# Optimization experiments

Hardware: AMD Instinct MI355X
Metric: run time of the kernel (lower is better)

## Reference

```python
import jax, jax.numpy as jnp
import numpy as np

B, S, D, H = 2, 2048, 2048, 16
DPH = D // H  # 128


def setup_inputs() -> dict:
    key = jax.random.key(0)
    k1, _ = jax.random.split(key)
    query = jax.random.normal(k1, (B, S, D), dtype=jnp.float32)
    mask = jnp.ones((B, S), dtype=jnp.int32)  # True = allow attention
    return {"query": query, "mask": mask}


def reference(query, mask):
    # Faithful to the given snippet: q_lin/k_lin/v_lin/out_lin are defined in
    # __init__ but never invoked in forward, and attn_mask is constructed but
    # never applied to dot_prod. Self-attention path: key = value = query.
    b, q_len, dim = query.shape
    scale = np.sqrt(DPH).astype(np.float32)

    # prepare_head: [B, S, D] -> [B, H, S, dph]
    q = query.reshape(b, q_len, H, DPH).transpose(0, 2, 1, 3) / scale
    k = query.reshape(b, q_len, H, DPH).transpose(0, 2, 1, 3)
    v = k

    # dot_prod = (q/scale) @ k^T : [B, H, Sq, Sk]
    dot_prod = jnp.einsum('bhqd,bhkd->bhqk', q, k)

    # fp32 softmax, cast back to query dtype (mask is NOT applied in source)
    attn_weights = jax.nn.softmax(dot_prod.astype(jnp.float32), axis=-1).astype(query.dtype)

    attentioned = jnp.einsum('bhqk,bhkd->bhqd', attn_weights, v)
    out = attentioned.transpose(0, 2, 1, 3).reshape(b, q_len, dim)

    # new_incr_state tensors (prev_key/prev_value in [B, H, S, dph], prev_mask)
    prev_key = k.reshape(b, H, q_len, DPH)
    prev_value = v.reshape(b, H, q_len, DPH)
    # dot_prod returned as [B*H, Sq, Sk] to match source shape
    return out, prev_key, prev_value, mask, dot_prod.reshape(b * H, q_len, q_len)
```

## Files before the change

kernel.cpp:

```cpp
#include <hip/hip_runtime.h>
#include <hip/hip_bf16.h>

#define BB 2
#define HH 16
#define SS 2048
#define DD 2048
#define DPH_ 128
#define QBLK 128
#define KBLK 64
#define NT (SS / KBLK)

#define KSTR 136
#define VSTR 72
#define PSTR 72

typedef __bf16 bf16x8 __attribute__((ext_vector_type(8)));
typedef unsigned short u16x8 __attribute__((ext_vector_type(8)));
typedef float f32x4 __attribute__((ext_vector_type(4)));

__device__ __forceinline__ unsigned f2bfbits32(float f) {
  unsigned u = __builtin_bit_cast(unsigned, f);
  u += 0x7FFFu + ((u >> 16) & 1u);
  return u >> 16;
}
__device__ __forceinline__ unsigned short f2bfbits(float f) {
  return (unsigned short)f2bfbits32(f);
}
__device__ __forceinline__ __bf16 f2bf(float f) {
  unsigned short s = f2bfbits(f);
  return __builtin_bit_cast(__bf16, s);
}
__device__ __forceinline__ void nt_store4(const float4& v, float* p) {
  f32x4 t = {v.x, v.y, v.z, v.w};
  __builtin_nontemporal_store(t, (f32x4*)p);
}

template <int CTRL>
__device__ __forceinline__ float dpp_addf(float x) {
  int y = __builtin_amdgcn_mov_dpp(__builtin_bit_cast(int, x), CTRL, 0xF, 0xF, true);
  return x + __builtin_bit_cast(float, y);
}
template <int CTRL>
__device__ __forceinline__ float dpp_maxf(float x) {
  int y = __builtin_amdgcn_mov_dpp(__builtin_bit_cast(int, x), CTRL, 0xF, 0xF, true);
  return fmaxf(x, __builtin_bit_cast(float, y));
}
__device__ __forceinline__ float dpp_sum16(float x) {
  x = dpp_addf<0xB1>(x);
  x = dpp_addf<0x4E>(x);
  x = dpp_addf<0x124>(x);
  x = dpp_addf<0x128>(x);
  return x;
}
__device__ __forceinline__ float dpp_max16(float x) {
  x = dpp_maxf<0xB1>(x);
  x = dpp_maxf<0x4E>(x);
  x = dpp_maxf<0x124>(x);
  x = dpp_maxf<0x128>(x);
  return x;
}

template <bool PRE>
__global__ __launch_bounds__(256)
void preproc(const float* __restrict__ q, const int* __restrict__ mask,
             __bf16* __restrict__ qb, float* __restrict__ omask) {
  const size_t i = (size_t)blockIdx.x * 256 + threadIdx.x;
  const size_t e = i * 8;
  if constexpr (PRE) {
    const float4 v0 = *(const float4*)(q + e);
    const float4 v1 = *(const float4*)(q + e + 4);
    u16x8 t;
    t[0] = f2bfbits(v0.x); t[1] = f2bfbits(v0.y);
    t[2] = f2bfbits(v0.z); t[3] = f2bfbits(v0.w);
    t[4] = f2bfbits(v1.x); t[5] = f2bfbits(v1.y);
    t[6] = f2bfbits(v1.z); t[7] = f2bfbits(v1.w);
    *(u16x8*)(qb + e) = t;
  }
  if (i < (size_t)BB * SS) omask[i] = (float)mask[i];
}

template <bool PRE>
__global__ __launch_bounds__(256, 2)
void attn_fused(const __bf16* __restrict__ qb, const float* __restrict__ qf,
                float* __restrict__ out, float* __restrict__ dot,
                float* __restrict__ pk, float* __restrict__ pv) {
  __shared__ __bf16 kls[KBLK * KSTR];
  __shared__ __bf16 vls[DPH_ * VSTR];
  __shared__ __bf16 pls[4 * 32 * PSTR];

  const int bid = blockIdx.x;
  const int xcd = bid & 7;
  const int t_  = bid >> 3;
  const int qt  = t_ & 15;
  const int G   = (t_ >> 4) * 8 + xcd;
  const int h   = G & 15;
  const int b   = G >> 4;

  const int tid  = threadIdx.x;
  const int wid  = tid >> 6;
  const int lane = tid & 63;
  const int g    = lane >> 4;
  const int c    = lane & 15;

  const int qbase = qt * QBLK;
  const float scale = 0.08838834764831845f;

  const size_t headoff = (size_t)b * SS * DD + (size_t)h * DPH_;
  const __bf16* qbh = PRE ? qb + headoff : nullptr;
  const float*  qfh = qf + headoff;

  bf16x8 aq[2][4];
  #pragma unroll
  for (int u = 0; u < 2; ++u) {
    const int row = qbase + wid * 32 + u * 16 + c;
    if constexpr (PRE) {
      const __bf16* p = qbh + (size_t)row * DD + 8 * g;
      #pragma unroll
      for (int st = 0; st < 4; ++st) aq[u][st] = *(const bf16x8*)(p + st * 32);
    } else {
      const float* p = qfh + (size_t)row * DD + 8 * g;
      #pragma unroll
      for (int st = 0; st < 4; ++st) {
        u16x8 t;
        #pragma unroll
        for (int i2 = 0; i2 < 8; ++i2) t[i2] = f2bfbits(p[st * 32 + i2]);
        aq[u][st] = __builtin_bit_cast(bf16x8, t);
      }
    }
  }

  const int p2 = tid & 31;
  const int oo = tid >> 5;
  const int r0 = 2 * p2;

  bf16x8 st0, st1, st2, st3;
  auto load_tile = [&](int kvb) {
    if constexpr (PRE) {
      const __bf16* pA = qbh + (size_t)(kvb + r0) * DD + 16 * oo;
      st0 = *(const bf16x8*)pA;
      st1 = *(const bf16x8*)(pA + 8);
      st2 = *(const bf16x8*)(pA + DD);
      st3 = *(const bf16x8*)(pA + DD + 8);
    } else {
      const float* pA = qfh + (size_t)(kvb + r0) * DD + 16 * oo;
      u16x8 t0, t1, t2, t3;
      #pragma unroll
      for (int i2 = 0; i2 < 8; ++i2) {
        t0[i2] = f2bfbits(pA[i2]);
        t1[i2] = f2bfbits(pA[8 + i2]);
        t2[i2] = f2bfbits(pA[DD + i2]);
        t3[i2] = f2bfbits(pA[DD + 8 + i2]);
      }
      st0 = __builtin_bit_cast(bf16x8, t0);
      st1 = __builtin_bit_cast(bf16x8, t1);
      st2 = __builtin_bit_cast(bf16x8, t2);
      st3 = __builtin_bit_cast(bf16x8, t3);
    }
  };
  auto write_tile = [&]() {
    *(bf16x8*)(&kls[r0 * KSTR + 16 * oo])       = st0;
    *(bf16x8*)(&kls[r0 * KSTR + 16 * oo + 8])   = st1;
    *(bf16x8*)(&kls[(r0+1) * KSTR + 16 * oo])     = st2;
    *(bf16x8*)(&kls[(r0+1) * KSTR + 16 * oo + 8]) = st3;
    const unsigned* a0 = (const unsigned*)&st0;
    const unsigned* a1 = (const unsigned*)&st1;
    const unsigned* b0 = (const unsigned*)&st2;
    const unsigned* b1 = (const unsigned*)&st3;
    #pragma unroll
    for (int j = 0; j < 8; ++j) {
      unsigned loA = (j < 4 ? a0[j] : a1[j - 4]);
      unsigned loB = (j < 4 ? b0[j] : b1[j - 4]);
      unsigned w0 = (loA & 0xFFFFu) | (loB << 16);
      unsigned w1 = (loA >> 16) | (loB & 0xFFFF0000u);
      *(unsigned*)(&vls[(16 * oo + 2 * j) * VSTR + r0]) = w0;
      *(unsigned*)(&vls[(16 * oo + 2 * j + 1) * VSTR + r0]) = w1;
    }
  };

  const f32x4 zero4 = {0.f, 0.f, 0.f, 0.f};
  f32x4 o[2][8];
  #pragma unroll
  for (int u = 0; u < 2; ++u)
    #pragma unroll
    for (int t = 0; t < 8; ++t) o[u][t] = zero4;
  float m[2][4], l[2][4];
  #pragma unroll
  for (int u = 0; u < 2; ++u)
    #pragma unroll
    for (int r = 0; r < 4; ++r) { m[u][r] = -1e30f; l[u][r] = 0.0f; }

  float* __restrict__ dotb = dot + ((size_t)(b * HH + h) << 22);

  load_tile(0);
  write_tile();
  __syncthreads();

  for (int kt = 0; kt < NT; ++kt) {
    const int kvbase = kt * KBLK;

    f32x4 s[2][4];
    #pragma unroll
    for (int u = 0; u < 2; ++u)
      #pragma unroll
      for (int ct = 0; ct < 4; ++ct) s[u][ct] = zero4;
    __builtin_amdgcn_s_setprio(1);
    #pragma unroll
    for (int st = 0; st < 4; ++st) {
      #pragma unroll
      for (int ct = 0; ct < 4; ++ct) {
        bf16x8 bk = *(const bf16x8*)(&kls[(ct * 16 + c) * KSTR + st * 32 + 8 * g]);
        #pragma unroll
        for (int u = 0; u < 2; ++u)
          s[u][ct] = __builtin_amdgcn_mfma_f32_16x16x32_bf16(aq[u][st], bk, s[u][ct], 0, 0, 0);
      }
    }
    __builtin_amdgcn_s_setprio(0);

    if (kt + 1 < NT) load_tile(kvbase + KBLK);

    #pragma unroll
    for (int u = 0; u < 2; ++u) {
      #pragma unroll
      for (int ct = 0; ct < 4; ++ct) s[u][ct] *= scale;
      #pragma unroll
      for (int r = 0; r < 4; ++r) {
        float* dp = dotb + (size_t)(qbase + wid * 32 + u * 16 + 4 * g + r) * SS + kvbase + c;
        #pragma unroll
        for (int ct = 0; ct < 4; ++ct)
          __builtin_nontemporal_store(s[u][ct][r], dp + ct * 16);
      }
    }

    #pragma unroll
    for (int u = 0; u < 2; ++u) {
      float mx[4];
      #pragma unroll
      for (int r = 0; r < 4; ++r) {
        float tm = fmaxf(fmaxf(s[u][0][r], s[u][1][r]), fmaxf(s[u][2][r], s[u][3][r]));
        mx[r] = dpp_max16(tm);
      }
      const bool need = (mx[0] > m[u][0] + 8.0f) | (mx[1] > m[u][1] + 8.0f) |
                        (mx[2] > m[u][2] + 8.0f) | (mx[3] > m[u][3] + 8.0f);
      if (__any(need)) {
        #pragma unroll
        for (int r = 0; r < 4; ++r) {
          const float mn = fmaxf(m[u][r], mx[r]);
          const float alpha = __expf(m[u][r] - mn);
          m[u][r] = mn;
          l[u][r] *= alpha;
          #pragma unroll
          for (int t = 0; t < 8; ++t) o[u][t][r] *= alpha;
        }
      }
      float rs[4] = {0.f, 0.f, 0.f, 0.f};
      #pragma unroll
      for (int ct = 0; ct < 4; ++ct) {
        #pragma unroll
        for (int r = 0; r < 4; ++r) {
          float p = __expf(s[u][ct][r] - m[u][r]);
          s[u][ct][r] = p;
          rs[r] += p;
        }
      }
      #pragma unroll
      for (int r = 0; r < 4; ++r)
        l[u][r] += dpp_sum16(rs[r]);
      __bf16* pw = &pls[wid * 32 * PSTR];
      #pragma unroll
      for (int ct = 0; ct < 4; ++ct)
        #pragma unroll
        for (int r = 0; r < 4; ++r)
          pw[(u * 16 + 4 * g + r) * PSTR + ct * 16 + c] = f2bf(s[u][ct][r]);
    }

    __builtin_amdgcn_s_setprio(1);
    #pragma unroll
    for (int kk = 0; kk < 2; ++kk) {
      bf16x8 ap[2];
      #pragma unroll
      for (int u = 0; u < 2; ++u)
        ap[u] = *(const bf16x8*)(&pls[wid * 32 * PSTR + (u * 16 + c) * PSTR + kk * 32 + 8 * g]);
      #pragma unroll
      for (int t = 0; t < 8; ++t) {
        bf16x8 bv = *(const bf16x8*)(&vls[(t * 16 + c) * VSTR + kk * 32 + 8 * g]);
        #pragma unroll
        for (int u = 0; u < 2; ++u)
          o[u][t] = __builtin_amdgcn_mfma_f32_16x16x32_bf16(ap[u], bv, o[u][t], 0, 0, 0);
      }
    }
    __builtin_amdgcn_s_setprio(0);

    __syncthreads();
    if (kt + 1 < NT) write_tile();
    __syncthreads();
  }

  #pragma unroll
  for (int u = 0; u < 2; ++u)
    #pragma unroll
    for (int r = 0; r < 4; ++r) {
      float inv = 1.0f / l[u][r];
      float* op = out + (size_t)(b * SS + qbase + wid * 32 + u * 16 + 4 * g + r) * DD + h * DPH_ + c;
      #pragma unroll
      for (int t = 0; t < 8; ++t)
        __builtin_nontemporal_store(o[u][t][r] * inv, op + t * 16);
    }

  {
    const size_t bh = (size_t)b * HH + h;
    const int col = (tid & 31) * 4;
    #pragma unroll
    for (int rr = 0; rr < 16; ++rr) {
      const int row = qbase + rr * 8 + (tid >> 5);
      const float4 v = *(const float4*)(qfh + (size_t)row * DD + col);
      nt_store4(v, pk + (bh * SS + row) * DPH_ + col);
      nt_store4(v, pv + (bh * SS + row) * DPH_ + col);
    }
  }
}

extern "C" void kernel_launch(void* const* d_in, const int* in_sizes, int n_in,
                              void* d_out, int out_size, void* d_ws, size_t ws_size,
                              hipStream_t stream) {
  const float* q    = (const float*)d_in[0];
  const int*   mask = (const int*)d_in[1];
  float* out = (float*)d_out;

  float* o_out  = out;
  float* o_pk   = out + 8388608;
  float* o_pv   = out + 16777216;
  float* o_mask = out + 25165824;
  float* o_dot  = out + 25169920;

  const size_t need = (size_t)BB * SS * DD * sizeof(__bf16);
  const dim3 agrid(512);

  if (ws_size >= need) {
    __bf16* qbf = (__bf16*)d_ws;
    preproc<true><<<4096, 256, 0, stream>>>(q, mask, qbf, o_mask);
    attn_fused<true><<<agrid, 256, 0, stream>>>(qbf, q, o_out, o_dot, o_pk, o_pv);
  } else {
    preproc<false><<<4096, 256, 0, stream>>>(q, mask, nullptr, o_mask);
    attn_fused<false><<<agrid, 256, 0, stream>>>(nullptr, q, o_out, o_dot, o_pk, o_pv);
  }
}
```

Before: 179.8 us.

## Double-buffer K/V LDS tiles and use 512-thread blocks covering 256 queries

Doubles the query tile to 256 rows per block with 8 waves (512 threads) and halves the grid, so each K/V tile loaded into LDS is shared by twice as many query rows. K and V shared buffers become double-buffered, which removes one __syncthreads per iteration because the next tile is written into the alternate buffer. The V transpose now uses scalar 16-bit LDS stores instead of packed 32-bit writes. With 256 blocks on a 256-CU part, there is roughly one block per CU, so latency hiding may get worse. The scalar LDS stores may also add bank conflicts.

```diff
diff --git a/kernel.cpp b/kernel.cpp
--- a/kernel.cpp
+++ b/kernel.cpp
@@ -6,7 +6,7 @@
 #define SS 2048
 #define DD 2048
 #define DPH_ 128
-#define QBLK 128
+#define QBLK 256
 #define KBLK 64
 #define NT (SS / KBLK)
 
@@ -80,19 +80,19 @@
 }
 
 template <bool PRE>
-__global__ __launch_bounds__(256, 2)
+__global__ __launch_bounds__(512, 2)
 void attn_fused(const __bf16* __restrict__ qb, const float* __restrict__ qf,
                 float* __restrict__ out, float* __restrict__ dot,
                 float* __restrict__ pk, float* __restrict__ pv) {
-  __shared__ __bf16 kls[KBLK * KSTR];
-  __shared__ __bf16 vls[DPH_ * VSTR];
-  __shared__ __bf16 pls[4 * 32 * PSTR];
+  __shared__ __align__(16) __bf16 kls[2][KBLK * KSTR];
+  __shared__ __align__(16) __bf16 vls[2][DPH_ * VSTR];
+  __shared__ __align__(16) __bf16 pls[8 * 32 * PSTR];
 
   const int bid = blockIdx.x;
   const int xcd = bid & 7;
-  const int t_  = bid >> 3;
-  const int qt  = t_ & 15;
-  const int G   = (t_ >> 4) * 8 + xcd;
+  const int idx = bid >> 3;
+  const int qt  = idx & 7;
+  const int G   = (idx >> 3) * 8 + xcd;
   const int h   = G & 15;
   const int b   = G >> 4;
 
@@ -129,51 +129,36 @@
     }
   }
 
-  const int p2 = tid & 31;
-  const int oo = tid >> 5;
-  const int r0 = 2 * p2;
-
-  bf16x8 st0, st1, st2, st3;
+  const int r0 = (tid & 31) * 2 + (tid >> 8);
+  const int oo = (tid >> 5) & 7;
+
+  bf16x8 st0, st1;
   auto load_tile = [&](int kvb) {
     if constexpr (PRE) {
       const __bf16* pA = qbh + (size_t)(kvb + r0) * DD + 16 * oo;
       st0 = *(const bf16x8*)pA;
       st1 = *(const bf16x8*)(pA + 8);
-      st2 = *(const bf16x8*)(pA + DD);
-      st3 = *(const bf16x8*)(pA + DD + 8);
     } else {
       const float* pA = qfh + (size_t)(kvb + r0) * DD + 16 * oo;
-      u16x8 t0, t1, t2, t3;
+      u16x8 t0, t1;
       #pragma unroll
       for (int i2 = 0; i2 < 8; ++i2) {
         t0[i2] = f2bfbits(pA[i2]);
         t1[i2] = f2bfbits(pA[8 + i2]);
-        t2[i2] = f2bfbits(pA[DD + i2]);
-        t3[i2] = f2bfbits(pA[DD + 8 + i2]);
       }
       st0 = __builtin_bit_cast(bf16x8, t0);
       st1 = __builtin_bit_cast(bf16x8, t1);
-      st2 = __builtin_bit_cast(bf16x8, t2);
-      st3 = __builtin_bit_cast(bf16x8, t3);
     }
   };
-  auto write_tile = [&]() {
-    *(bf16x8*)(&kls[r0 * KSTR + 16 * oo])       = st0;
-    *(bf16x8*)(&kls[r0 * KSTR + 16 * oo + 8])   = st1;
-    *(bf16x8*)(&kls[(r0+1) * KSTR + 16 * oo])     = st2;
-    *(bf16x8*)(&kls[(r0+1) * KSTR + 16 * oo + 8]) = st3;
-    const unsigned* a0 = (const unsigned*)&st0;
-    const unsigned* a1 = (const unsigned*)&st1;
-    const unsigned* b0 = (const unsigned*)&st2;
-    const unsigned* b1 = (const unsigned*)&st3;
+  auto write_tile = [&](int bufi) {
+    __bf16* kb = kls[bufi];
+    __bf16* vb = vls[bufi];
+    *(bf16x8*)(&kb[r0 * KSTR + 16 * oo])     = st0;
+    *(bf16x8*)(&kb[r0 * KSTR + 16 * oo + 8]) = st1;
     #pragma unroll
     for (int j = 0; j < 8; ++j) {
-      unsigned loA = (j < 4 ? a0[j] : a1[j - 4]);
-      unsigned loB = (j < 4 ? b0[j] : b1[j - 4]);
-      unsigned w0 = (loA & 0xFFFFu) | (loB << 16);
-      unsigned w1 = (loA >> 16) | (loB & 0xFFFF0000u);
-      *(unsigned*)(&vls[(16 * oo + 2 * j) * VSTR + r0]) = w0;
-      *(unsigned*)(&vls[(16 * oo + 2 * j + 1) * VSTR + r0]) = w1;
+      vb[(16 * oo + j) * VSTR + r0]     = st0[j];
+      vb[(16 * oo + 8 + j) * VSTR + r0] = st1[j];
     }
   };
 
@@ -192,11 +177,12 @@
   float* __restrict__ dotb = dot + ((size_t)(b * HH + h) << 22);
 
   load_tile(0);
-  write_tile();
+  write_tile(0);
   __syncthreads();
 
   for (int kt = 0; kt < NT; ++kt) {
     const int kvbase = kt * KBLK;
+    const int cur = kt & 1;
 
     f32x4 s[2][4];
     #pragma unroll
@@ -208,7 +194,7 @@
     for (int st = 0; st < 4; ++st) {
       #pragma unroll
       for (int ct = 0; ct < 4; ++ct) {
-        bf16x8 bk = *(const bf16x8*)(&kls[(ct * 16 + c) * KSTR + st * 32 + 8 * g]);
+        bf16x8 bk = *(const bf16x8*)(&kls[cur][(ct * 16 + c) * KSTR + st * 32 + 8 * g]);
         #pragma unroll
         for (int u = 0; u < 2; ++u)
           s[u][ct] = __builtin_amdgcn_mfma_f32_16x16x32_bf16(aq[u][st], bk, s[u][ct], 0, 0, 0);
@@ -282,7 +268,7 @@
         ap[u] = *(const bf16x8*)(&pls[wid * 32 * PSTR + (u * 16 + c) * PSTR + kk * 32 + 8 * g]);
       #pragma unroll
       for (int t = 0; t < 8; ++t) {
-        bf16x8 bv = *(const bf16x8*)(&vls[(t * 16 + c) * VSTR + kk * 32 + 8 * g]);
+        bf16x8 bv = *(const bf16x8*)(&vls[cur][(t * 16 + c) * VSTR + kk * 32 + 8 * g]);
         #pragma unroll
         for (int u = 0; u < 2; ++u)
           o[u][t] = __builtin_amdgcn_mfma_f32_16x16x32_bf16(ap[u], bv, o[u][t], 0, 0, 0);
@@ -290,8 +276,7 @@
     }
     __builtin_amdgcn_s_setprio(0);
 
-    __syncthreads();
-    if (kt + 1 < NT) write_tile();
+    if (kt + 1 < NT) write_tile(cur ^ 1);
     __syncthreads();
   }
 
@@ -311,7 +296,7 @@
     const int col = (tid & 31) * 4;
     #pragma unroll
     for (int rr = 0; rr < 16; ++rr) {
-      const int row = qbase + rr * 8 + (tid >> 5);
+      const int row = qbase + rr * 16 + (tid >> 5);
       const float4 v = *(const float4*)(qfh + (size_t)row * DD + col);
       nt_store4(v, pk + (bh * SS + row) * DPH_ + col);
       nt_store4(v, pv + (bh * SS + row) * DPH_ + col);
@@ -333,14 +318,14 @@
   float* o_dot  = out + 25169920;
 
   const size_t need = (size_t)BB * SS * DD * sizeof(__bf16);
-  const dim3 agrid(512);
+  const dim3 agrid(256);
 
   if (ws_size >= need) {
     __bf16* qbf = (__bf16*)d_ws;
     preproc<true><<<4096, 256, 0, stream>>>(q, mask, qbf, o_mask);
-    attn_fused<true><<<agrid, 256, 0, stream>>>(qbf, q, o_out, o_dot, o_pk, o_pv);
+    attn_fused<true><<<agrid, 512, 0, stream>>>(qbf, q, o_out, o_dot, o_pk, o_pv);
   } else {
     preproc<false><<<4096, 256, 0, stream>>>(q, mask, nullptr, o_mask);
-    attn_fused<false><<<agrid, 256, 0, stream>>>(nullptr, q, o_out, o_dot, o_pk, o_pv);
-  }
-}
+    attn_fused<false><<<agrid, 512, 0, stream>>>(nullptr, q, o_out, o_dot, o_pk, o_pv);
+  }
+}
```

New measurement: 186.2 us. 1.04x slower.
